# Optimization experiments

Hardware: AMD Instinct MI355X
Metric: run time of the kernel (lower is better)

Reference implementation:

```python
import jax, jax.numpy as jnp
import numpy as np

N_NODES = 100000
N_EDGES = 1600000
IN_DIM, HIDDEN, OUT = 256, 128, 64


def setup_inputs() -> dict:
    key = jax.random.key(0)
    k1, k2, k3, k4 = jax.random.split(key, 4)
    x = jax.random.normal(k1, (N_NODES, IN_DIM), dtype=jnp.float32)
    edge_index = jax.random.randint(k2, (2, N_EDGES), 0, N_NODES, dtype=jnp.int32)
    # glorot-ish init for the GCN linear layers
    W1 = jax.random.normal(k3, (IN_DIM, HIDDEN), dtype=jnp.float32) / np.sqrt(IN_DIM)
    b1 = jnp.zeros((HIDDEN,), dtype=jnp.float32)
    W2 = jax.random.normal(k4, (HIDDEN, OUT), dtype=jnp.float32) / np.sqrt(HIDDEN)
    b2 = jnp.zeros((OUT,), dtype=jnp.float32)
    return {"x": x, "edge_index": edge_index, "W1": W1, "b1": b1, "W2": W2, "b2": b2}


def gcn_layer(x, src, dst, W, b):
    """PyG GCNConv: add self-loops, symmetric deg^-1/2 normalization,
    linear transform, scatter-add aggregation, bias."""
    h = x @ W  # [N, F_out]
    # degree over self-looped graph: in-degree(dst counts) + 1 self loop
    deg = jax.ops.segment_sum(jnp.ones((src.shape[0],), h.dtype), dst,
                              num_segments=N_NODES) + 1.0
    dinv = jax.lax.rsqrt(deg)  # [N]
    coef = dinv[src] * dinv[dst]  # [E]
    agg = jax.ops.segment_sum(h[src] * coef[:, None], dst, num_segments=N_NODES)
    # self-loop contribution (norm = dinv[i]^2) without materializing loop edges
    agg = agg + h * (dinv * dinv)[:, None]
    return agg + b


def reference(x, edge_index, W1, b1, W2, b2):
    src, dst = edge_index[0], edge_index[1]
    h = jax.nn.relu(gcn_layer(x, src, dst, W1, b1))
    return jax.nn.relu(gcn_layer(h, src, dst, W2, b2))
```

## Files before the change

### kernel.cpp

```cpp
#include <hip/hip_runtime.h>

#define N_NODES 100000
#define N_EDGES 1600000
#define IN_DIM 256
#define HIDDEN 128
#define OUT_DIM 64

#define NBIN 391
#define NBLK3 256
#define CHUNK 6250
#define NMAT (NBIN * NBLK3)
#define NBLK_SCAN (NMAT / 256)
#define CAP 6144

typedef __bf16 bf16x8 __attribute__((ext_vector_type(8)));
typedef __bf16 bf16x4 __attribute__((ext_vector_type(4)));
typedef float f32x4 __attribute__((ext_vector_type(4)));

__launch_bounds__(256)
__global__ void k_hist(const int* __restrict__ dst, int* __restrict__ cnt2) {
    __shared__ int hist[NBIN];
    for (int i = threadIdx.x; i < NBIN; i += 256) hist[i] = 0;
    __syncthreads();
    int base = blockIdx.x * CHUNK;
    for (int i = threadIdx.x; i < CHUNK; i += 256)
        atomicAdd(&hist[dst[base + i] >> 8], 1);
    __syncthreads();
    for (int k = threadIdx.x; k < NBIN; k += 256)
        cnt2[k * NBLK3 + blockIdx.x] = hist[k];
}

__global__ void k_scan1(int* __restrict__ a, int* __restrict__ bsum) {
    __shared__ int tmp[256];
    int t = threadIdx.x;
    int i = blockIdx.x * 256 + t;
    int v = a[i];
    tmp[t] = v;
    __syncthreads();
    #pragma unroll
    for (int off = 1; off < 256; off <<= 1) {
        int p = (t >= off) ? tmp[t - off] : 0;
        __syncthreads();
        tmp[t] += p;
        __syncthreads();
    }
    a[i] = tmp[t] - v;
    if (t == 255) bsum[blockIdx.x] = tmp[255];
}

__global__ void k_scan2(int* __restrict__ bsum) {
    __shared__ int tmp[512];
    int t = threadIdx.x;
    int v = (t < NBLK_SCAN) ? bsum[t] : 0;
    tmp[t] = v;
    __syncthreads();
    #pragma unroll
    for (int off = 1; off < 512; off <<= 1) {
        int p = (t >= off) ? tmp[t - off] : 0;
        __syncthreads();
        tmp[t] += p;
        __syncthreads();
    }
    if (t < NBLK_SCAN) bsum[t] = tmp[t] - v;
}

__global__ void k_scan3(int* __restrict__ a, const int* __restrict__ bsum) {
    int i = blockIdx.x * 256 + threadIdx.x;
    a[i] += bsum[blockIdx.x];
}

__launch_bounds__(256)
__global__ void k_scatter_bins(const int* __restrict__ src, const int* __restrict__ dst,
                               const int* __restrict__ off2,
                               unsigned int* __restrict__ ebuf) {
    __shared__ int cursor[NBIN];
    for (int k = threadIdx.x; k < NBIN; k += 256)
        cursor[k] = off2[k * NBLK3 + blockIdx.x];
    __syncthreads();
    int base = blockIdx.x * CHUNK;
    for (int i = threadIdx.x; i < CHUNK; i += 256) {
        int s = src[base + i], d = dst[base + i];
        int pos = atomicAdd(&cursor[d >> 8], 1);
        ebuf[pos] = ((unsigned)s << 8) | (unsigned)(d & 255);
    }
}

__launch_bounds__(256)
__global__ void k_fine(const unsigned int* __restrict__ ebuf, const int* __restrict__ off2,
                       int* __restrict__ esrc, int* __restrict__ rowstart,
                       float* __restrict__ dinv) {
    __shared__ int hist[256];
    __shared__ int tmp[256];
    __shared__ int nodeoff[256];
    __shared__ int cursor[256];
    __shared__ unsigned int ed[CAP];
    __shared__ int sOut[CAP];

    const int k = blockIdx.x;
    const int t = threadIdx.x;
    const int e0 = off2[k * NBLK3];
    const int e1 = (k + 1 < NBIN) ? off2[(k + 1) * NBLK3] : N_EDGES;
    int m = e1 - e0;
    if (m > CAP) m = CAP;

    hist[t] = 0;
    __syncthreads();
    for (int i = t; i < m; i += 256) {
        unsigned v = ebuf[e0 + i];
        ed[i] = v;
        atomicAdd(&hist[v & 255], 1);
    }
    __syncthreads();

    int v = hist[t];
    tmp[t] = v;
    __syncthreads();
    #pragma unroll
    for (int off = 1; off < 256; off <<= 1) {
        int p = (t >= off) ? tmp[t - off] : 0;
        __syncthreads();
        tmp[t] += p;
        __syncthreads();
    }
    nodeoff[t] = tmp[t] - v;
    cursor[t] = tmp[t] - v;
    __syncthreads();

    for (int i = t; i < m; i += 256) {
        unsigned e = ed[i];
        int pos = atomicAdd(&cursor[e & 255], 1);
        sOut[pos] = (int)(e >> 8);
    }
    __syncthreads();

    for (int i = t; i < m; i += 256) esrc[e0 + i] = sOut[i];

    int n = k * 256 + t;
    if (n < N_NODES) {
        rowstart[n] = e0 + nodeoff[t];
        dinv[n] = rsqrtf((float)hist[t] + 1.0f);
    }
    if (k == 0 && t == 0) rowstart[N_NODES] = N_EDGES;
}

__device__ __forceinline__ int bsw1(int c, int kk) {
    return c * 256 + (kk ^ ((c & 7) << 3));
}

__launch_bounds__(512, 4)
__global__ void k_gemm1(const float* __restrict__ X, const float* __restrict__ W1,
                        __bf16* __restrict__ H) {
    __shared__ __attribute__((aligned(16))) __bf16 Bs[128 * 256];

    const int t = threadIdx.x;
    const int wave = t >> 6;
    const int lane = t & 63;
    const int lm = lane & 15;
    const int q = lane >> 4;
    const int row0 = blockIdx.x * 256;

    for (int p = 0; p < 8; ++p) {
        int i = t + 512 * p;
        int c = i & 127;
        int kg = i >> 7;
        float v[8];
        #pragma unroll
        for (int j = 0; j < 8; ++j)
            v[j] = W1[(kg * 8 + j) * HIDDEN + c];
        bf16x8 w;
        #pragma unroll
        for (int j = 0; j < 8; ++j) w[j] = (__bf16)v[j];
        *(bf16x8*)&Bs[bsw1(c, kg * 8)] = w;
    }
    __syncthreads();

    f32x4 acc[2][8] = {};

    #pragma unroll
    for (int k0 = 0; k0 < IN_DIM; k0 += 32) {
        bf16x8 af[2];
        #pragma unroll
        for (int mi = 0; mi < 2; ++mi) {
            int g = row0 + wave * 32 + mi * 16 + lm;
            float4 v0 = make_float4(0.f, 0.f, 0.f, 0.f), v1 = v0;
            if (g < N_NODES) {
                const float* p = &X[(size_t)g * IN_DIM + k0 + q * 8];
                v0 = *(const float4*)p;
                v1 = *(const float4*)(p + 4);
            }
            bf16x8 a;
            a[0] = (__bf16)v0.x; a[1] = (__bf16)v0.y;
            a[2] = (__bf16)v0.z; a[3] = (__bf16)v0.w;
            a[4] = (__bf16)v1.x; a[5] = (__bf16)v1.y;
            a[6] = (__bf16)v1.z; a[7] = (__bf16)v1.w;
            af[mi] = a;
        }
        #pragma unroll
        for (int ni = 0; ni < 8; ++ni) {
            bf16x8 bfr = *(const bf16x8*)&Bs[bsw1(ni * 16 + lm, k0 + q * 8)];
            #pragma unroll
            for (int mi = 0; mi < 2; ++mi)
                acc[mi][ni] = __builtin_amdgcn_mfma_f32_16x16x32_bf16(
                    af[mi], bfr, acc[mi][ni], 0, 0, 0);
        }
    }

    #pragma unroll
    for (int mi = 0; mi < 2; ++mi) {
        #pragma unroll
        for (int r = 0; r < 4; ++r) {
            int grow = row0 + wave * 32 + mi * 16 + q * 4 + r;
            if (grow < N_NODES) {
                #pragma unroll
                for (int ni = 0; ni < 8; ++ni)
                    H[grow * HIDDEN + ni * 16 + lm] = (__bf16)acc[mi][ni][r];
            }
        }
    }
}

__launch_bounds__(256)
__global__ void k_gather1(const int* __restrict__ rowstart, const int* __restrict__ esrc,
                          const float* __restrict__ dinv,
                          const __bf16* __restrict__ H, const float* __restrict__ b1,
                          __bf16* __restrict__ AGG) {
    int n = blockIdx.x * 16 + (threadIdx.x >> 4);
    if (n >= N_NODES) return;
    int j = (threadIdx.x & 15) * 8;

    float dn = dinv[n];
    float s = dn * dn;
    bf16x8 h = *(const bf16x8*)&H[n * HIDDEN + j];
    float acc[8];
    #pragma unroll
    for (int i = 0; i < 8; ++i) acc[i] = (float)h[i] * s;

    int p0 = rowstart[n], p1 = rowstart[n + 1];
    int p = p0;
    for (; p + 3 < p1; p += 4) {
        int s0 = esrc[p + 0], s1 = esrc[p + 1], s2 = esrc[p + 2], s3 = esrc[p + 3];
        float c0 = dinv[s0] * dn, c1 = dinv[s1] * dn;
        float c2 = dinv[s2] * dn, c3 = dinv[s3] * dn;
        bf16x8 v0 = *(const bf16x8*)&H[s0 * HIDDEN + j];
        bf16x8 v1 = *(const bf16x8*)&H[s1 * HIDDEN + j];
        bf16x8 v2 = *(const bf16x8*)&H[s2 * HIDDEN + j];
        bf16x8 v3 = *(const bf16x8*)&H[s3 * HIDDEN + j];
        #pragma unroll
        for (int i = 0; i < 8; ++i) acc[i] = fmaf((float)v0[i], c0, acc[i]);
        #pragma unroll
        for (int i = 0; i < 8; ++i) acc[i] = fmaf((float)v1[i], c1, acc[i]);
        #pragma unroll
        for (int i = 0; i < 8; ++i) acc[i] = fmaf((float)v2[i], c2, acc[i]);
        #pragma unroll
        for (int i = 0; i < 8; ++i) acc[i] = fmaf((float)v3[i], c3, acc[i]);
    }
    for (; p < p1; ++p) {
        int sidx = esrc[p];
        float c = dinv[sidx] * dn;
        bf16x8 v = *(const bf16x8*)&H[sidx * HIDDEN + j];
        #pragma unroll
        for (int i = 0; i < 8; ++i) acc[i] = fmaf((float)v[i], c, acc[i]);
    }

    float4 bb0 = *(const float4*)&b1[j];
    float4 bb1 = *(const float4*)&b1[j + 4];
    bf16x8 o;
    o[0] = (__bf16)fmaxf(acc[0] + bb0.x, 0.f);
    o[1] = (__bf16)fmaxf(acc[1] + bb0.y, 0.f);
    o[2] = (__bf16)fmaxf(acc[2] + bb0.z, 0.f);
    o[3] = (__bf16)fmaxf(acc[3] + bb0.w, 0.f);
    o[4] = (__bf16)fmaxf(acc[4] + bb1.x, 0.f);
    o[5] = (__bf16)fmaxf(acc[5] + bb1.y, 0.f);
    o[6] = (__bf16)fmaxf(acc[6] + bb1.z, 0.f);
    o[7] = (__bf16)fmaxf(acc[7] + bb1.w, 0.f);
    *(bf16x8*)&AGG[n * HIDDEN + j] = o;
}

__device__ __forceinline__ int bsw2(int c, int kk) {
    return c * 128 + (kk ^ ((c & 7) << 3));
}

__launch_bounds__(512, 4)
__global__ void k_gemm2(const __bf16* __restrict__ AGG, const float* __restrict__ W2,
                        __bf16* __restrict__ H2) {
    __shared__ __attribute__((aligned(16))) __bf16 Bs[64 * 128];

    const int t = threadIdx.x;
    const int wave = t >> 6;
    const int lane = t & 63;
    const int lm = lane & 15;
    const int q = lane >> 4;
    const int row0 = blockIdx.x * 256;

    for (int p = 0; p < 2; ++p) {
        int i = t + 512 * p;
        int c = i & 63;
        int kg = i >> 6;
        float v[8];
        #pragma unroll
        for (int j = 0; j < 8; ++j)
            v[j] = W2[(kg * 8 + j) * OUT_DIM + c];
        bf16x8 w;
        #pragma unroll
        for (int j = 0; j < 8; ++j) w[j] = (__bf16)v[j];
        *(bf16x8*)&Bs[bsw2(c, kg * 8)] = w;
    }
    __syncthreads();

    f32x4 acc[2][4] = {};

    #pragma unroll
    for (int k0 = 0; k0 < HIDDEN; k0 += 32) {
        bf16x8 af[2];
        #pragma unroll
        for (int mi = 0; mi < 2; ++mi) {
            int g = row0 + wave * 32 + mi * 16 + lm;
            bf16x8 a = {};
            if (g < N_NODES)
                a = *(const bf16x8*)&AGG[(size_t)g * HIDDEN + k0 + q * 8];
            af[mi] = a;
        }
        #pragma unroll
        for (int ni = 0; ni < 4; ++ni) {
            bf16x8 bfr = *(const bf16x8*)&Bs[bsw2(ni * 16 + lm, k0 + q * 8)];
            #pragma unroll
            for (int mi = 0; mi < 2; ++mi)
                acc[mi][ni] = __builtin_amdgcn_mfma_f32_16x16x32_bf16(
                    af[mi], bfr, acc[mi][ni], 0, 0, 0);
        }
    }

    #pragma unroll
    for (int mi = 0; mi < 2; ++mi) {
        #pragma unroll
        for (int r = 0; r < 4; ++r) {
            int grow = row0 + wave * 32 + mi * 16 + q * 4 + r;
            if (grow < N_NODES) {
                #pragma unroll
                for (int ni = 0; ni < 4; ++ni)
                    H2[grow * OUT_DIM + ni * 16 + lm] = (__bf16)acc[mi][ni][r];
            }
        }
    }
}

__launch_bounds__(256)
__global__ void k_gather2(const int* __restrict__ rowstart, const int* __restrict__ esrc,
                          const float* __restrict__ dinv,
                          const __bf16* __restrict__ H2, const float* __restrict__ b2,
                          float* __restrict__ OUT) {
    int n = blockIdx.x * 32 + (threadIdx.x >> 3);
    if (n >= N_NODES) return;
    int j = (threadIdx.x & 7) * 8;

    float dn = dinv[n];
    float s = dn * dn;
    bf16x8 h = *(const bf16x8*)&H2[n * OUT_DIM + j];
    float acc[8];
    #pragma unroll
    for (int i = 0; i < 8; ++i) acc[i] = (float)h[i] * s;

    int p0 = rowstart[n], p1 = rowstart[n + 1];
    int p = p0;
    for (; p + 3 < p1; p += 4) {
        int s0 = esrc[p + 0], s1 = esrc[p + 1], s2 = esrc[p + 2], s3 = esrc[p + 3];
        float c0 = dinv[s0] * dn, c1 = dinv[s1] * dn;
        float c2 = dinv[s2] * dn, c3 = dinv[s3] * dn;
        bf16x8 v0 = *(const bf16x8*)&H2[s0 * OUT_DIM + j];
        bf16x8 v1 = *(const bf16x8*)&H2[s1 * OUT_DIM + j];
        bf16x8 v2 = *(const bf16x8*)&H2[s2 * OUT_DIM + j];
        bf16x8 v3 = *(const bf16x8*)&H2[s3 * OUT_DIM + j];
        #pragma unroll
        for (int i = 0; i < 8; ++i) acc[i] = fmaf((float)v0[i], c0, acc[i]);
        #pragma unroll
        for (int i = 0; i < 8; ++i) acc[i] = fmaf((float)v1[i], c1, acc[i]);
        #pragma unroll
        for (int i = 0; i < 8; ++i) acc[i] = fmaf((float)v2[i], c2, acc[i]);
        #pragma unroll
        for (int i = 0; i < 8; ++i) acc[i] = fmaf((float)v3[i], c3, acc[i]);
    }
    for (; p < p1; ++p) {
        int sidx = esrc[p];
        float c = dinv[sidx] * dn;
        bf16x8 v = *(const bf16x8*)&H2[sidx * OUT_DIM + j];
        #pragma unroll
        for (int i = 0; i < 8; ++i) acc[i] = fmaf((float)v[i], c, acc[i]);
    }

    float4 bb0 = *(const float4*)&b2[j];
    float4 bb1 = *(const float4*)&b2[j + 4];
    float4 o0, o1;
    o0.x = fmaxf(acc[0] + bb0.x, 0.f);
    o0.y = fmaxf(acc[1] + bb0.y, 0.f);
    o0.z = fmaxf(acc[2] + bb0.z, 0.f);
    o0.w = fmaxf(acc[3] + bb0.w, 0.f);
    o1.x = fmaxf(acc[4] + bb1.x, 0.f);
    o1.y = fmaxf(acc[5] + bb1.y, 0.f);
    o1.z = fmaxf(acc[6] + bb1.z, 0.f);
    o1.w = fmaxf(acc[7] + bb1.w, 0.f);
    *(float4*)&OUT[n * OUT_DIM + j] = o0;
    *(float4*)&OUT[n * OUT_DIM + j + 4] = o1;
}

extern "C" void kernel_launch(void* const* d_in, const int* in_sizes, int n_in,
                              void* d_out, int out_size, void* d_ws, size_t ws_size,
                              hipStream_t stream) {
    const float* x  = (const float*)d_in[0];
    const int* ei   = (const int*)d_in[1];
    const float* W1 = (const float*)d_in[2];
    const float* b1 = (const float*)d_in[3];
    const float* W2 = (const float*)d_in[4];
    const float* b2 = (const float*)d_in[5];
    float* out = (float*)d_out;

    const int* src = ei;
    const int* dst = ei + N_EDGES;

    char* ws = (char*)d_ws;
    int*          cnt2     = (int*)         (ws + 0x000000);
    int*          bsum     = (int*)         (ws + 0x080000);
    int*          rowstart = (int*)         (ws + 0x090000);
    float*        dinv     = (float*)       (ws + 0x100000);
    unsigned int* ebuf     = (unsigned int*)(ws + 0x180000);
    int*          esrc     = (int*)         (ws + 0x800000);
    __bf16*       h1       = (__bf16*)      (ws + 0xE80000);
    __bf16*       agg1     = (__bf16*)      (ws + 0x2880000);
    __bf16*       h2       = (__bf16*)      (ws + 0x4280000);

    k_hist<<<NBLK3, 256, 0, stream>>>(dst, cnt2);
    k_scan1<<<NBLK_SCAN, 256, 0, stream>>>(cnt2, bsum);
    k_scan2<<<1, 512, 0, stream>>>(bsum);
    k_scan3<<<NBLK_SCAN, 256, 0, stream>>>(cnt2, bsum);
    k_scatter_bins<<<NBLK3, 256, 0, stream>>>(src, dst, cnt2, ebuf);
    k_fine<<<NBIN, 256, 0, stream>>>(ebuf, cnt2, esrc, rowstart, dinv);

    k_gemm1<<<(N_NODES + 255) / 256, 512, 0, stream>>>(x, W1, h1);
    k_gather1<<<(N_NODES + 15) / 16, 256, 0, stream>>>(rowstart, esrc, dinv, h1, b1, agg1);
    k_gemm2<<<(N_NODES + 255) / 256, 512, 0, stream>>>(agg1, W2, h2);
    k_gather2<<<(N_NODES + 31) / 32, 256, 0, stream>>>(rowstart, esrc, dinv, h2, b2, out);
}
```

Before: 335.2 us.

## Store hidden features in 16-column planes so gathers hit smaller L2 working sets

```diff
diff --git a/kernel.cpp b/kernel.cpp
--- a/kernel.cpp
+++ b/kernel.cpp
@@ -12,6 +12,8 @@
 #define NMAT (NBIN * NBLK3)
 #define NBLK_SCAN (NMAT / 256)
 #define CAP 6144
+
+#define PLANE (N_NODES * 16)
 
 typedef __bf16 bf16x8 __attribute__((ext_vector_type(8)));
 typedef __bf16 bf16x4 __attribute__((ext_vector_type(4)));
@@ -213,7 +215,7 @@
             if (grow < N_NODES) {
                 #pragma unroll
                 for (int ni = 0; ni < 8; ++ni)
-                    H[grow * HIDDEN + ni * 16 + lm] = (__bf16)acc[mi][ni][r];
+                    H[(size_t)ni * PLANE + grow * 16 + lm] = (__bf16)acc[mi][ni][r];
             }
         }
     }
@@ -224,16 +226,21 @@
                           const float* __restrict__ dinv,
                           const __bf16* __restrict__ H, const float* __restrict__ b1,
                           __bf16* __restrict__ AGG) {
-    int n = blockIdx.x * 16 + (threadIdx.x >> 4);
+    const int s  = blockIdx.x & 7;
+    const int nb = blockIdx.x >> 3;
+    const int ln = threadIdx.x >> 1;
+    const int f0 = (threadIdx.x & 1) * 8;
+    int n = nb * 128 + ln;
     if (n >= N_NODES) return;
-    int j = (threadIdx.x & 15) * 8;
+
+    const __bf16* Hs = H + (size_t)s * PLANE;
 
     float dn = dinv[n];
-    float s = dn * dn;
-    bf16x8 h = *(const bf16x8*)&H[n * HIDDEN + j];
+    float sc = dn * dn;
+    bf16x8 h = *(const bf16x8*)&Hs[n * 16 + f0];
     float acc[8];
     #pragma unroll
-    for (int i = 0; i < 8; ++i) acc[i] = (float)h[i] * s;
+    for (int i = 0; i < 8; ++i) acc[i] = (float)h[i] * sc;
 
     int p0 = rowstart[n], p1 = rowstart[n + 1];
     int p = p0;
@@ -241,10 +248,10 @@
         int s0 = esrc[p + 0], s1 = esrc[p + 1], s2 = esrc[p + 2], s3 = esrc[p + 3];
         float c0 = dinv[s0] * dn, c1 = dinv[s1] * dn;
         float c2 = dinv[s2] * dn, c3 = dinv[s3] * dn;
-        bf16x8 v0 = *(const bf16x8*)&H[s0 * HIDDEN + j];
-        bf16x8 v1 = *(const bf16x8*)&H[s1 * HIDDEN + j];
-        bf16x8 v2 = *(const bf16x8*)&H[s2 * HIDDEN + j];
-        bf16x8 v3 = *(const bf16x8*)&H[s3 * HIDDEN + j];
+        bf16x8 v0 = *(const bf16x8*)&Hs[s0 * 16 + f0];
+        bf16x8 v1 = *(const bf16x8*)&Hs[s1 * 16 + f0];
+        bf16x8 v2 = *(const bf16x8*)&Hs[s2 * 16 + f0];
+        bf16x8 v3 = *(const bf16x8*)&Hs[s3 * 16 + f0];
         #pragma unroll
         for (int i = 0; i < 8; ++i) acc[i] = fmaf((float)v0[i], c0, acc[i]);
         #pragma unroll
@@ -257,23 +264,16 @@
     for (; p < p1; ++p) {
         int sidx = esrc[p];
         float c = dinv[sidx] * dn;
-        bf16x8 v = *(const bf16x8*)&H[sidx * HIDDEN + j];
+        bf16x8 v = *(const bf16x8*)&Hs[sidx * 16 + f0];
         #pragma unroll
         for (int i = 0; i < 8; ++i) acc[i] = fmaf((float)v[i], c, acc[i]);
     }
 
-    float4 bb0 = *(const float4*)&b1[j];
-    float4 bb1 = *(const float4*)&b1[j + 4];
+    const float* bs = &b1[s * 16 + f0];
     bf16x8 o;
-    o[0] = (__bf16)fmaxf(acc[0] + bb0.x, 0.f);
-    o[1] = (__bf16)fmaxf(acc[1] + bb0.y, 0.f);
-    o[2] = (__bf16)fmaxf(acc[2] + bb0.z, 0.f);
-    o[3] = (__bf16)fmaxf(acc[3] + bb0.w, 0.f);
-    o[4] = (__bf16)fmaxf(acc[4] + bb1.x, 0.f);
-    o[5] = (__bf16)fmaxf(acc[5] + bb1.y, 0.f);
-    o[6] = (__bf16)fmaxf(acc[6] + bb1.z, 0.f);
-    o[7] = (__bf16)fmaxf(acc[7] + bb1.w, 0.f);
-    *(bf16x8*)&AGG[n * HIDDEN + j] = o;
+    #pragma unroll
+    for (int i = 0; i < 8; ++i) o[i] = (__bf16)fmaxf(acc[i] + bs[i], 0.f);
+    *(bf16x8*)&AGG[(size_t)s * PLANE + n * 16 + f0] = o;
 }
 
 __device__ __forceinline__ int bsw2(int c, int kk) {
@@ -316,8 +316,11 @@
         for (int mi = 0; mi < 2; ++mi) {
             int g = row0 + wave * 32 + mi * 16 + lm;
             bf16x8 a = {};
-            if (g < N_NODES)
-                a = *(const bf16x8*)&AGG[(size_t)g * HIDDEN + k0 + q * 8];
+            if (g < N_NODES) {
+                int c = (k0 >> 3) + q;
+                const __bf16* Ap = AGG + (size_t)(c >> 1) * PLANE;
+                a = *(const bf16x8*)&Ap[(size_t)g * 16 + (c & 1) * 8];
+            }
             af[mi] = a;
         }
         #pragma unroll
@@ -338,7 +341,7 @@
             if (grow < N_NODES) {
                 #pragma unroll
                 for (int ni = 0; ni < 4; ++ni)
-                    H2[grow * OUT_DIM + ni * 16 + lm] = (__bf16)acc[mi][ni][r];
+                    H2[(size_t)ni * PLANE + grow * 16 + lm] = (__bf16)acc[mi][ni][r];
             }
         }
     }
@@ -349,16 +352,23 @@
                           const float* __restrict__ dinv,
                           const __bf16* __restrict__ H2, const float* __restrict__ b2,
                           float* __restrict__ OUT) {
-    int n = blockIdx.x * 32 + (threadIdx.x >> 3);
+    const int l   = blockIdx.x & 7;
+    const int s4  = l & 3;
+    const int nb2 = blockIdx.x >> 3;
+    const int node_block = nb2 * 2 + (l >> 2);
+    const int ln = threadIdx.x >> 1;
+    const int f0 = (threadIdx.x & 1) * 8;
+    int n = node_block * 128 + ln;
     if (n >= N_NODES) return;
-    int j = (threadIdx.x & 7) * 8;
+
+    const __bf16* Hs = H2 + (size_t)s4 * PLANE;
 
     float dn = dinv[n];
-    float s = dn * dn;
-    bf16x8 h = *(const bf16x8*)&H2[n * OUT_DIM + j];
+    float sc = dn * dn;
+    bf16x8 h = *(const bf16x8*)&Hs[n * 16 + f0];
     float acc[8];
     #pragma unroll
-    for (int i = 0; i < 8; ++i) acc[i] = (float)h[i] * s;
+    for (int i = 0; i < 8; ++i) acc[i] = (float)h[i] * sc;
 
     int p0 = rowstart[n], p1 = rowstart[n + 1];
     int p = p0;
@@ -366,10 +376,10 @@
         int s0 = esrc[p + 0], s1 = esrc[p + 1], s2 = esrc[p + 2], s3 = esrc[p + 3];
         float c0 = dinv[s0] * dn, c1 = dinv[s1] * dn;
         float c2 = dinv[s2] * dn, c3 = dinv[s3] * dn;
-        bf16x8 v0 = *(const bf16x8*)&H2[s0 * OUT_DIM + j];
-        bf16x8 v1 = *(const bf16x8*)&H2[s1 * OUT_DIM + j];
-        bf16x8 v2 = *(const bf16x8*)&H2[s2 * OUT_DIM + j];
-        bf16x8 v3 = *(const bf16x8*)&H2[s3 * OUT_DIM + j];
+        bf16x8 v0 = *(const bf16x8*)&Hs[s0 * 16 + f0];
+        bf16x8 v1 = *(const bf16x8*)&Hs[s1 * 16 + f0];
+        bf16x8 v2 = *(const bf16x8*)&Hs[s2 * 16 + f0];
+        bf16x8 v3 = *(const bf16x8*)&Hs[s3 * 16 + f0];
         #pragma unroll
         for (int i = 0; i < 8; ++i) acc[i] = fmaf((float)v0[i], c0, acc[i]);
         #pragma unroll
@@ -382,24 +392,24 @@
     for (; p < p1; ++p) {
         int sidx = esrc[p];
         float c = dinv[sidx] * dn;
-        bf16x8 v = *(const bf16x8*)&H2[sidx * OUT_DIM + j];
+        bf16x8 v = *(const bf16x8*)&Hs[sidx * 16 + f0];
         #pragma unroll
         for (int i = 0; i < 8; ++i) acc[i] = fmaf((float)v[i], c, acc[i]);
     }
 
-    float4 bb0 = *(const float4*)&b2[j];
-    float4 bb1 = *(const float4*)&b2[j + 4];
+    const float* bs = &b2[s4 * 16 + f0];
     float4 o0, o1;
-    o0.x = fmaxf(acc[0] + bb0.x, 0.f);
-    o0.y = fmaxf(acc[1] + bb0.y, 0.f);
-    o0.z = fmaxf(acc[2] + bb0.z, 0.f);
-    o0.w = fmaxf(acc[3] + bb0.w, 0.f);
-    o1.x = fmaxf(acc[4] + bb1.x, 0.f);
-    o1.y = fmaxf(acc[5] + bb1.y, 0.f);
-    o1.z = fmaxf(acc[6] + bb1.z, 0.f);
-    o1.w = fmaxf(acc[7] + bb1.w, 0.f);
-    *(float4*)&OUT[n * OUT_DIM + j] = o0;
-    *(float4*)&OUT[n * OUT_DIM + j + 4] = o1;
+    o0.x = fmaxf(acc[0] + bs[0], 0.f);
+    o0.y = fmaxf(acc[1] + bs[1], 0.f);
+    o0.z = fmaxf(acc[2] + bs[2], 0.f);
+    o0.w = fmaxf(acc[3] + bs[3], 0.f);
+    o1.x = fmaxf(acc[4] + bs[4], 0.f);
+    o1.y = fmaxf(acc[5] + bs[5], 0.f);
+    o1.z = fmaxf(acc[6] + bs[6], 0.f);
+    o1.w = fmaxf(acc[7] + bs[7], 0.f);
+    float* op = &OUT[(size_t)n * OUT_DIM + s4 * 16 + f0];
+    *(float4*)op = o0;
+    *(float4*)(op + 4) = o1;
 }
 
 extern "C" void kernel_launch(void* const* d_in, const int* in_sizes, int n_in,
@@ -435,7 +445,7 @@
     k_fine<<<NBIN, 256, 0, stream>>>(ebuf, cnt2, esrc, rowstart, dinv);
 
     k_gemm1<<<(N_NODES + 255) / 256, 512, 0, stream>>>(x, W1, h1);
-    k_gather1<<<(N_NODES + 15) / 16, 256, 0, stream>>>(rowstart, esrc, dinv, h1, b1, agg1);
+    k_gather1<<<((N_NODES + 127) / 128) * 8, 256, 0, stream>>>(rowstart, esrc, dinv, h1, b1, agg1);
     k_gemm2<<<(N_NODES + 255) / 256, 512, 0, stream>>>(agg1, W2, h2);
-    k_gather2<<<(N_NODES + 31) / 32, 256, 0, stream>>>(rowstart, esrc, dinv, h2, b2, out);
-}
+    k_gather2<<<((N_NODES + 255) / 256) * 8, 256, 0, stream>>>(rowstart, esrc, dinv, h2, b2, out);
+}
```

Result: slower. 460.1 us (+37.2%).

## Fold scan block offsets into consumers and halve GEMM row tiles

Applied to the files above, without the earlier changes.

```diff
diff --git a/kernel.cpp b/kernel.cpp
--- a/kernel.cpp
+++ b/kernel.cpp
@@ -64,18 +64,13 @@
     if (t < NBLK_SCAN) bsum[t] = tmp[t] - v;
 }
 
-__global__ void k_scan3(int* __restrict__ a, const int* __restrict__ bsum) {
-    int i = blockIdx.x * 256 + threadIdx.x;
-    a[i] += bsum[blockIdx.x];
-}
-
 __launch_bounds__(256)
 __global__ void k_scatter_bins(const int* __restrict__ src, const int* __restrict__ dst,
-                               const int* __restrict__ off2,
+                               const int* __restrict__ off2, const int* __restrict__ bsum,
                                unsigned int* __restrict__ ebuf) {
     __shared__ int cursor[NBIN];
     for (int k = threadIdx.x; k < NBIN; k += 256)
-        cursor[k] = off2[k * NBLK3 + blockIdx.x];
+        cursor[k] = off2[k * NBLK3 + blockIdx.x] + bsum[k];
     __syncthreads();
     int base = blockIdx.x * CHUNK;
     for (int i = threadIdx.x; i < CHUNK; i += 256) {
@@ -87,6 +82,7 @@
 
 __launch_bounds__(256)
 __global__ void k_fine(const unsigned int* __restrict__ ebuf, const int* __restrict__ off2,
+                       const int* __restrict__ bsum,
                        int* __restrict__ esrc, int* __restrict__ rowstart,
                        float* __restrict__ dinv) {
     __shared__ int hist[256];
@@ -98,8 +94,8 @@
 
     const int k = blockIdx.x;
     const int t = threadIdx.x;
-    const int e0 = off2[k * NBLK3];
-    const int e1 = (k + 1 < NBIN) ? off2[(k + 1) * NBLK3] : N_EDGES;
+    const int e0 = off2[k * NBLK3] + bsum[k];
+    const int e1 = (k + 1 < NBIN) ? off2[(k + 1) * NBLK3] + bsum[k + 1] : N_EDGES;
     int m = e1 - e0;
     if (m > CAP) m = CAP;
 
@@ -143,48 +139,47 @@
     if (k == 0 && t == 0) rowstart[N_NODES] = N_EDGES;
 }
 
-__device__ __forceinline__ int bsw1(int c, int kk) {
-    return c * 256 + (kk ^ ((c & 7) << 3));
+__device__ __forceinline__ int bsw1h(int c, int kk) {
+    return c * 128 + (kk ^ ((c & 7) << 3));
 }
 
 __launch_bounds__(512, 4)
 __global__ void k_gemm1(const float* __restrict__ X, const float* __restrict__ W1,
                         __bf16* __restrict__ H) {
-    __shared__ __attribute__((aligned(16))) __bf16 Bs[128 * 256];
+    __shared__ __attribute__((aligned(16))) __bf16 Bs[128 * 128];
 
     const int t = threadIdx.x;
     const int wave = t >> 6;
     const int lane = t & 63;
     const int lm = lane & 15;
     const int q = lane >> 4;
-    const int row0 = blockIdx.x * 256;
-
-    for (int p = 0; p < 8; ++p) {
-        int i = t + 512 * p;
-        int c = i & 127;
-        int kg = i >> 7;
-        float v[8];
-        #pragma unroll
-        for (int j = 0; j < 8; ++j)
-            v[j] = W1[(kg * 8 + j) * HIDDEN + c];
-        bf16x8 w;
-        #pragma unroll
-        for (int j = 0; j < 8; ++j) w[j] = (__bf16)v[j];
-        *(bf16x8*)&Bs[bsw1(c, kg * 8)] = w;
-    }
-    __syncthreads();
-
-    f32x4 acc[2][8] = {};
-
-    #pragma unroll
-    for (int k0 = 0; k0 < IN_DIM; k0 += 32) {
-        bf16x8 af[2];
-        #pragma unroll
-        for (int mi = 0; mi < 2; ++mi) {
-            int g = row0 + wave * 32 + mi * 16 + lm;
+    const int row0 = blockIdx.x * 128;
+    const int g = row0 + wave * 16 + lm;
+
+    f32x4 acc[8] = {};
+
+    for (int half = 0; half < 2; ++half) {
+        __syncthreads();
+        for (int p = 0; p < 4; ++p) {
+            int i = t + 512 * p;
+            int c = i & 127;
+            int kg = i >> 7;
+            float v[8];
+            #pragma unroll
+            for (int j = 0; j < 8; ++j)
+                v[j] = W1[(half * 128 + kg * 8 + j) * HIDDEN + c];
+            bf16x8 w;
+            #pragma unroll
+            for (int j = 0; j < 8; ++j) w[j] = (__bf16)v[j];
+            *(bf16x8*)&Bs[bsw1h(c, kg * 8)] = w;
+        }
+        __syncthreads();
+
+        #pragma unroll
+        for (int k0 = 0; k0 < 128; k0 += 32) {
             float4 v0 = make_float4(0.f, 0.f, 0.f, 0.f), v1 = v0;
             if (g < N_NODES) {
-                const float* p = &X[(size_t)g * IN_DIM + k0 + q * 8];
+                const float* p = &X[(size_t)g * IN_DIM + half * 128 + k0 + q * 8];
                 v0 = *(const float4*)p;
                 v1 = *(const float4*)(p + 4);
             }
@@ -193,28 +188,21 @@
             a[2] = (__bf16)v0.z; a[3] = (__bf16)v0.w;
             a[4] = (__bf16)v1.x; a[5] = (__bf16)v1.y;
             a[6] = (__bf16)v1.z; a[7] = (__bf16)v1.w;
-            af[mi] = a;
+            #pragma unroll
+            for (int ni = 0; ni < 8; ++ni) {
+                bf16x8 bfr = *(const bf16x8*)&Bs[bsw1h(ni * 16 + lm, k0 + q * 8)];
+                acc[ni] = __builtin_amdgcn_mfma_f32_16x16x32_bf16(a, bfr, acc[ni], 0, 0, 0);
+            }
         }
-        #pragma unroll
-        for (int ni = 0; ni < 8; ++ni) {
-            bf16x8 bfr = *(const bf16x8*)&Bs[bsw1(ni * 16 + lm, k0 + q * 8)];
+    }
+
+    #pragma unroll
+    for (int r = 0; r < 4; ++r) {
+        int grow = row0 + wave * 16 + q * 4 + r;
+        if (grow < N_NODES) {
             #pragma unroll
-            for (int mi = 0; mi < 2; ++mi)
-                acc[mi][ni] = __builtin_amdgcn_mfma_f32_16x16x32_bf16(
-                    af[mi], bfr, acc[mi][ni], 0, 0, 0);
-        }
-    }
-
-    #pragma unroll
-    for (int mi = 0; mi < 2; ++mi) {
-        #pragma unroll
-        for (int r = 0; r < 4; ++r) {
-            int grow = row0 + wave * 32 + mi * 16 + q * 4 + r;
-            if (grow < N_NODES) {
-                #pragma unroll
-                for (int ni = 0; ni < 8; ++ni)
-                    H[grow * HIDDEN + ni * 16 + lm] = (__bf16)acc[mi][ni][r];
-            }
+            for (int ni = 0; ni < 8; ++ni)
+                H[grow * HIDDEN + ni * 16 + lm] = (__bf16)acc[ni][r];
         }
     }
 }
@@ -280,7 +268,7 @@
     return c * 128 + (kk ^ ((c & 7) << 3));
 }
 
-__launch_bounds__(512, 4)
+__launch_bounds__(512, 8)
 __global__ void k_gemm2(const __bf16* __restrict__ AGG, const float* __restrict__ W2,
                         __bf16* __restrict__ H2) {
     __shared__ __attribute__((aligned(16))) __bf16 Bs[64 * 128];
@@ -290,7 +278,8 @@
     const int lane = t & 63;
     const int lm = lane & 15;
     const int q = lane >> 4;
-    const int row0 = blockIdx.x * 256;
+    const int row0 = blockIdx.x * 128;
+    const int g = row0 + wave * 16 + lm;
 
     for (int p = 0; p < 2; ++p) {
         int i = t + 512 * p;
@@ -307,39 +296,27 @@
     }
     __syncthreads();
 
-    f32x4 acc[2][4] = {};
+    f32x4 acc[4] = {};
 
     #pragma unroll
     for (int k0 = 0; k0 < HIDDEN; k0 += 32) {
-        bf16x8 af[2];
-        #pragma unroll
-        for (int mi = 0; mi < 2; ++mi) {
-            int g = row0 + wave * 32 + mi * 16 + lm;
-            bf16x8 a = {};
-            if (g < N_NODES)
-                a = *(const bf16x8*)&AGG[(size_t)g * HIDDEN + k0 + q * 8];
-            af[mi] = a;
-        }
+        bf16x8 a = {};
+        if (g < N_NODES)
+            a = *(const bf16x8*)&AGG[(size_t)g * HIDDEN + k0 + q * 8];
         #pragma unroll
         for (int ni = 0; ni < 4; ++ni) {
             bf16x8 bfr = *(const bf16x8*)&Bs[bsw2(ni * 16 + lm, k0 + q * 8)];
+            acc[ni] = __builtin_amdgcn_mfma_f32_16x16x32_bf16(a, bfr, acc[ni], 0, 0, 0);
+        }
+    }
+
+    #pragma unroll
+    for (int r = 0; r < 4; ++r) {
+        int grow = row0 + wave * 16 + q * 4 + r;
+        if (grow < N_NODES) {
             #pragma unroll
-            for (int mi = 0; mi < 2; ++mi)
-                acc[mi][ni] = __builtin_amdgcn_mfma_f32_16x16x32_bf16(
-                    af[mi], bfr, acc[mi][ni], 0, 0, 0);
-        }
-    }
-
-    #pragma unroll
-    for (int mi = 0; mi < 2; ++mi) {
-        #pragma unroll
-        for (int r = 0; r < 4; ++r) {
-            int grow = row0 + wave * 32 + mi * 16 + q * 4 + r;
-            if (grow < N_NODES) {
-                #pragma unroll
-                for (int ni = 0; ni < 4; ++ni)
-                    H2[grow * OUT_DIM + ni * 16 + lm] = (__bf16)acc[mi][ni][r];
-            }
+            for (int ni = 0; ni < 4; ++ni)
+                H2[grow * OUT_DIM + ni * 16 + lm] = (__bf16)acc[ni][r];
         }
     }
 }
@@ -430,12 +407,11 @@
     k_hist<<<NBLK3, 256, 0, stream>>>(dst, cnt2);
     k_scan1<<<NBLK_SCAN, 256, 0, stream>>>(cnt2, bsum);
     k_scan2<<<1, 512, 0, stream>>>(bsum);
-    k_scan3<<<NBLK_SCAN, 256, 0, stream>>>(cnt2, bsum);
-    k_scatter_bins<<<NBLK3, 256, 0, stream>>>(src, dst, cnt2, ebuf);
-    k_fine<<<NBIN, 256, 0, stream>>>(ebuf, cnt2, esrc, rowstart, dinv);
-
-    k_gemm1<<<(N_NODES + 255) / 256, 512, 0, stream>>>(x, W1, h1);
+    k_scatter_bins<<<NBLK3, 256, 0, stream>>>(src, dst, cnt2, bsum, ebuf);
+    k_fine<<<NBIN, 256, 0, stream>>>(ebuf, cnt2, bsum, esrc, rowstart, dinv);
+
+    k_gemm1<<<(N_NODES + 127) / 128, 512, 0, stream>>>(x, W1, h1);
     k_gather1<<<(N_NODES + 15) / 16, 256, 0, stream>>>(rowstart, esrc, dinv, h1, b1, agg1);
-    k_gemm2<<<(N_NODES + 255) / 256, 512, 0, stream>>>(agg1, W2, h2);
+    k_gemm2<<<(N_NODES + 127) / 128, 512, 0, stream>>>(agg1, W2, h2);
     k_gather2<<<(N_NODES + 31) / 32, 256, 0, stream>>>(rowstart, esrc, dinv, h2, b2, out);
 }
```

Measured after the change: 335.8 us. About the same (+0.2%).
